# Kernel tuning notes

Measured on AMD Instinct MI355X. Metric: run time of the kernel, lower is better.

The kernel has to match this reference:

```python
import jax, jax.numpy as jnp
import numpy as np

V, E = 50000, 800000
NODE_IN, EDGE_IN, OUT, HEADS = 128, 16, 32, 4
NEG_SLOPE = 0.2  # DGL EdgeGATConv default negative_slope


def setup_inputs() -> dict:
    key = jax.random.key(0)
    ks = jax.random.split(key, 10)
    return {
        "node_feats": jax.random.normal(ks[0], (V, NODE_IN), jnp.float32),
        "edge_feats": jax.random.normal(ks[1], (E, EDGE_IN), jnp.float32),
        "src": jax.random.randint(ks[2], (E,), 0, V),
        "dst": jax.random.randint(ks[3], (E,), 0, V),
        "W_node": jax.random.normal(ks[4], (NODE_IN, HEADS * OUT), jnp.float32) * 0.05,
        "W_edge": jax.random.normal(ks[5], (EDGE_IN, HEADS * OUT), jnp.float32) * 0.05,
        "attn_l": jax.random.normal(ks[6], (HEADS, OUT), jnp.float32) * 0.05,
        "attn_r": jax.random.normal(ks[7], (HEADS, OUT), jnp.float32) * 0.05,
        "attn_e": jax.random.normal(ks[8], (HEADS, OUT), jnp.float32) * 0.05,
        "res_W": jax.random.normal(ks[9], (NODE_IN, HEADS * OUT), jnp.float32) * 0.05,
        "bias": jnp.zeros((HEADS * OUT,), jnp.float32),
    }


def _leaky_relu(x, slope):
    return jnp.where(x >= 0, x, slope * x)


def reference(node_feats, edge_feats, src, dst, W_node, W_edge, attn_l, attn_r, attn_e, res_W, bias):
    V = node_feats.shape[0]
    H, F = attn_l.shape
    # linear projections
    ft = (node_feats @ W_node).reshape(V, H, F)    # [V,H,F]
    fe = (edge_feats @ W_edge).reshape(-1, H, F)   # [E,H,F]
    # per-head attention logits
    el = jnp.einsum('vhf,hf->vh', ft, attn_l)      # [V,H]
    er = jnp.einsum('vhf,hf->vh', ft, attn_r)      # [V,H]
    ee = jnp.einsum('ehf,hf->eh', fe, attn_e)      # [E,H]
    e = _leaky_relu(el[src] + er[dst] + ee, NEG_SLOPE)  # [E,H]
    # edge softmax over incoming edges of each destination node (stable)
    emax = jax.ops.segment_max(e, dst, num_segments=V)  # [V,H]
    ex = jnp.exp(e - emax[dst])
    esum = jax.ops.segment_sum(ex, dst, num_segments=V)  # [V,H]
    a = ex / esum[dst]                                   # [E,H]
    # weighted message passing: u_mul_e(ft, a) then sum to dst
    msg = ft[src] * a[:, :, None]                        # [E,H,F]
    rst = jax.ops.segment_sum(msg, dst, num_segments=V)  # [V,H,F]
    # residual connection + bias (EdgeGATConv residual=True, bias=True)
    rst = rst + (node_feats @ res_W).reshape(V, H, F)
    rst = rst + bias.reshape(1, H, F)
    # agg_mode='flatten': concat heads
    return rst.reshape(V, H * F)
```

## Files before the change

kernel.cpp:

```cpp
#include <hip/hip_runtime.h>
#include <hip/hip_fp16.h>
#include <cstdint>

#define V_N 50000
#define E_N 800000
#define NODE_IN 128
#define EDGE_IN 16
#define HF 128
#define NEG_SLOPE 0.2f
#define NB_SCAN 196

#define OFF_FT    0
#define OFF_EL    3200000
#define OFF_ER    3400000
#define OFF_DEG   3600000
#define OFF_ROW   3650000
#define OFF_BSUM  3700004
#define OFF_RANK  3700260
#define OFF_REC   4500260
#define OFF_WATT  7700260
#define OFF_BFRAG 7700324

typedef short bf16x8 __attribute__((ext_vector_type(8)));
typedef float f32x4 __attribute__((ext_vector_type(4)));

__device__ __forceinline__ unsigned short f2bf(float f) {
    unsigned u = __float_as_uint(f);
    u += 0x7fffu + ((u >> 16) & 1u);
    return (unsigned short)(u >> 16);
}
__device__ __forceinline__ unsigned pk2(float lo, float hi) {
    return (unsigned)f2bf(lo) | ((unsigned)f2bf(hi) << 16);
}
__device__ __forceinline__ float bflo(unsigned w) { return __uint_as_float(w << 16); }
__device__ __forceinline__ float bfhi(unsigned w) { return __uint_as_float(w & 0xffff0000u); }

typedef __fp16 fp16x2 __attribute__((ext_vector_type(2)));
__device__ __forceinline__ unsigned pkh2(float a, float b) {
    fp16x2 h = __builtin_amdgcn_cvt_pkrtz(a, b);
    return __builtin_bit_cast(unsigned, h);
}
__device__ __forceinline__ __half2 u2h(unsigned u) {
    return __builtin_bit_cast(__half2, u);
}
__device__ __forceinline__ unsigned h2u(__half2 h) {
    return __builtin_bit_cast(unsigned, h);
}

__global__ void k_prep(const float* __restrict__ We,
                       const float* __restrict__ attn_e,
                       const float* __restrict__ Wn,
                       const float* __restrict__ Wr,
                       float* __restrict__ watt,
                       unsigned* __restrict__ bfrag,
                       int* __restrict__ deg) {
    int g = blockIdx.x * 256 + threadIdx.x;
    for (int i = g; i < V_N; i += 16384) deg[i] = 0;
    if (blockIdx.x == 0 && threadIdx.x < 64) {
        int k = threadIdx.x >> 2, h = threadIdx.x & 3;
        float s = 0.f;
        #pragma unroll
        for (int f = 0; f < 32; f++)
            s += We[k * HF + h * 32 + f] * attn_e[h * 32 + f];
        watt[k * 4 + h] = s;
    }
    if (g < 16384) {
        int c    = g >> 8;
        int lane = (g >> 2) & 63;
        int jp   = g & 3;
        int nt = c >> 2, ks = c & 3;
        int col = nt * 16 + (lane & 15);
        int k   = ks * 32 + (lane >> 4) * 8 + jp * 2;
        const float* W = (col < 128) ? Wn : Wr;
        int cc = col & 127;
        float x0 = W[(size_t)k * 128 + cc];
        float x1 = W[(size_t)(k + 1) * 128 + cc];
        bfrag[g] = pk2(x0, x1);
    }
}

__global__ __launch_bounds__(256) void k_node(
    const float* __restrict__ nf, const unsigned* __restrict__ bfragw,
    const float* __restrict__ attn_l, const float* __restrict__ attn_r,
    const float* __restrict__ bias,
    unsigned short* __restrict__ ftw, float* __restrict__ el,
    float* __restrict__ er, float* __restrict__ out)
{
    __shared__ __align__(16) float sSf[32 * 140];
    unsigned short* sA = (unsigned short*)sSf;

    const int t = threadIdx.x;
    const int lane = t & 63;
    const int w = t >> 6;
    const int nb = blockIdx.x * 32;
    const int n15 = lane & 15;
    const int q = lane >> 4;
    const unsigned short* bfrag = (const unsigned short*)bfragw;

    #pragma unroll
    for (int i = 0; i < 4; i++) {
        int f = t + i * 256;
        int node = f >> 5;
        int kc = (f & 31) * 4;
        float4 v = {0.f, 0.f, 0.f, 0.f};
        if (nb + node < V_N)
            v = *(const float4*)(nf + (size_t)(nb + node) * NODE_IN + kc);
        uint2 u2 = make_uint2(pk2(v.x, v.y), pk2(v.z, v.w));
        *(uint2*)&sA[node * 136 + kc] = u2;
    }
    __syncthreads();

    f32x4 acc[2][4];
    #pragma unroll
    for (int m = 0; m < 2; m++)
        #pragma unroll
        for (int tt = 0; tt < 4; tt++) acc[m][tt] = (f32x4){0.f, 0.f, 0.f, 0.f};

    #pragma unroll
    for (int ks = 0; ks < 4; ks++) {
        bf16x8 a0 = *(const bf16x8*)&sA[n15 * 136 + ks * 32 + q * 8];
        bf16x8 a1 = *(const bf16x8*)&sA[(16 + n15) * 136 + ks * 32 + q * 8];
        #pragma unroll
        for (int tt = 0; tt < 4; tt++) {
            int nt = w * 4 + tt;
            bf16x8 b = *(const bf16x8*)(bfrag + ((size_t)(nt * 4 + ks) * 64 + lane) * 8);
            acc[0][tt] = __builtin_amdgcn_mfma_f32_16x16x32_bf16(a0, b, acc[0][tt], 0, 0, 0);
            acc[1][tt] = __builtin_amdgcn_mfma_f32_16x16x32_bf16(a1, b, acc[1][tt], 0, 0, 0);
        }
    }

    if (w < 2) {
        #pragma unroll
        for (int hh = 0; hh < 2; hh++) {
            int head = w * 2 + hh;
            float al0 = attn_l[head * 32 + n15];
            float al1 = attn_l[head * 32 + 16 + n15];
            float ar0 = attn_r[head * 32 + n15];
            float ar1 = attn_r[head * 32 + 16 + n15];
            #pragma unroll
            for (int m = 0; m < 2; m++) {
                #pragma unroll
                for (int r = 0; r < 4; r++) {
                    float fa = acc[m][hh * 2][r], fb = acc[m][hh * 2 + 1][r];
                    float elp = fa * al0 + fb * al1;
                    float erp = fa * ar0 + fb * ar1;
                    elp += __shfl_xor(elp, 1); erp += __shfl_xor(erp, 1);
                    elp += __shfl_xor(elp, 2); erp += __shfl_xor(erp, 2);
                    elp += __shfl_xor(elp, 4); erp += __shfl_xor(erp, 4);
                    elp += __shfl_xor(elp, 8); erp += __shfl_xor(erp, 8);
                    int node = nb + m * 16 + q * 4 + r;
                    if (n15 == 0 && node < V_N) {
                        el[node * 4 + head] = elp;
                        er[node * 4 + head] = erp;
                    }
                }
            }
        }
        #pragma unroll
        for (int m = 0; m < 2; m++)
            #pragma unroll
            for (int r = 0; r < 4; r++) {
                int node = nb + m * 16 + q * 4 + r;
                if (node < V_N) {
                    uint2 u;
                    u.x = pkh2(acc[m][0][r], acc[m][1][r]);
                    u.y = pkh2(acc[m][2][r], acc[m][3][r]);
                    *(uint2*)(ftw + (size_t)node * 128 + w * 64 + n15 * 4) = u;
                }
            }
    }
    __syncthreads();

    if (w >= 2) {
        #pragma unroll
        for (int m = 0; m < 2; m++)
            #pragma unroll
            for (int tt = 0; tt < 4; tt++)
                #pragma unroll
                for (int r = 0; r < 4; r++)
                    sSf[(m * 16 + q * 4 + r) * 140 + (w - 2) * 64 + tt * 16 + n15] =
                        acc[m][tt][r];
    }
    __syncthreads();
    #pragma unroll
    for (int i = 0; i < 4; i++) {
        int u = t + i * 256;
        int node = u >> 5, c4 = (u & 31) * 4;
        if (nb + node < V_N) {
            float4 v = *(float4*)&sSf[node * 140 + c4];
            float4 b4 = *(const float4*)(bias + c4);
            v.x += b4.x; v.y += b4.y; v.z += b4.z; v.w += b4.w;
            *(float4*)(out + (size_t)(nb + node) * HF + c4) = v;
        }
    }
}

__global__ void k_hist(const int* __restrict__ dst, int* __restrict__ deg,
                       int* __restrict__ rank) {
    int e = blockIdx.x * 256 + threadIdx.x;
    if (e < E_N) rank[e] = atomicAdd(&deg[dst[e]], 1);
}

__global__ __launch_bounds__(256) void k_scan1(const int* __restrict__ deg,
                                               int* __restrict__ rowp,
                                               int* __restrict__ bsum) {
    __shared__ int sh[256];
    int t = threadIdx.x, b = blockIdx.x;
    int i = b * 256 + t;
    int v = (i < V_N) ? deg[i] : 0;
    sh[t] = v;
    __syncthreads();
    #pragma unroll
    for (int off = 1; off < 256; off <<= 1) {
        int u = (t >= off) ? sh[t - off] : 0;
        __syncthreads();
        sh[t] += u;
        __syncthreads();
    }
    if (i < V_N) rowp[i] = sh[t] - v;
    if (t == 255) bsum[b] = sh[255];
}

__global__ __launch_bounds__(256) void k_scan23(int* __restrict__ rowp,
                                                const int* __restrict__ bsum) {
    __shared__ int sh[256];
    int t = threadIdx.x, b = blockIdx.x;
    int v = (t < NB_SCAN) ? bsum[t] : 0;
    sh[t] = v;
    __syncthreads();
    #pragma unroll
    for (int off = 1; off < 256; off <<= 1) {
        int u = (t >= off) ? sh[t - off] : 0;
        __syncthreads();
        sh[t] += u;
        __syncthreads();
    }
    int boff = (b == 0) ? 0 : sh[b - 1];
    int i = b * 256 + t;
    if (i < V_N) rowp[i] += boff;
    if (i == 0) rowp[V_N] = E_N;
}

__global__ __launch_bounds__(256) void k_escatter(
    const float* __restrict__ ef, const int* __restrict__ src,
    const int* __restrict__ dst, const int* __restrict__ rank,
    const int* __restrict__ rowp, const float* __restrict__ watt,
    uint4* __restrict__ rec)
{
    __shared__ float sw[64];
    if (threadIdx.x < 64) sw[threadIdx.x] = watt[threadIdx.x];
    __syncthreads();
    int e = blockIdx.x * 256 + threadIdx.x;
    if (e >= E_N) return;

    float eev[4] = {0.f, 0.f, 0.f, 0.f};
    #pragma unroll
    for (int kq = 0; kq < 4; kq++) {
        float4 v = *(const float4*)(ef + (size_t)e * EDGE_IN + kq * 4);
        float vv[4] = {v.x, v.y, v.z, v.w};
        #pragma unroll
        for (int j = 0; j < 4; j++) {
            int k = kq * 4 + j;
            #pragma unroll
            for (int h = 0; h < 4; h++) eev[h] += vv[j] * sw[k * 4 + h];
        }
    }
    int d = dst[e];
    int p = rowp[d] + rank[e];
    uint4 r;
    r.x = (unsigned)src[e];
    r.y = pk2(eev[0], eev[1]);
    r.z = pk2(eev[2], eev[3]);
    r.w = 0;
    rec[p] = r;
}

__global__ __launch_bounds__(256) void k_gather(
    const int* __restrict__ row, const uint4* __restrict__ rec,
    const float* __restrict__ el, const float* __restrict__ er,
    const unsigned short* __restrict__ ftw, float* __restrict__ out)
{
    __shared__ unsigned aw[4][64][4];
    const int lane = threadIdx.x & 63;
    const int wid  = threadIdx.x >> 6;
    const int d = blockIdx.x * 4 + wid;
    if (d >= V_N) return;
    const int n0 = row[d];
    const int deg = row[d + 1] - n0;
    if (deg == 0) return;

    float4 er4 = *(const float4*)(er + (size_t)d * 4);

    int   si0 = 0;
    float4 ex0 = {0.f, 0.f, 0.f, 0.f};
    float4 s4  = {0.f, 0.f, 0.f, 0.f};
    for (int i = lane; i < deg; i += 64) {
        uint4 r = rec[n0 + i];
        float4 el4 = *(const float4*)(el + (size_t)r.x * 4);
        float x0 = el4.x + er4.x + bflo(r.y);
        float x1 = el4.y + er4.y + bfhi(r.y);
        float x2 = el4.z + er4.z + bflo(r.z);
        float x3 = el4.w + er4.w + bfhi(r.z);
        x0 = x0 >= 0.f ? x0 : NEG_SLOPE * x0;
        x1 = x1 >= 0.f ? x1 : NEG_SLOPE * x1;
        x2 = x2 >= 0.f ? x2 : NEG_SLOPE * x2;
        x3 = x3 >= 0.f ? x3 : NEG_SLOPE * x3;
        float4 ex = {__expf(x0), __expf(x1), __expf(x2), __expf(x3)};
        if (i == lane) { si0 = (int)r.x; ex0 = ex; }
        s4.x += ex.x; s4.y += ex.y; s4.z += ex.z; s4.w += ex.w;
    }
    #pragma unroll
    for (int off = 1; off < 64; off <<= 1) {
        s4.x += __shfl_xor(s4.x, off);
        s4.y += __shfl_xor(s4.y, off);
        s4.z += __shfl_xor(s4.z, off);
        s4.w += __shfl_xor(s4.w, off);
    }
    float4 rs4 = {1.f / s4.x, 1.f / s4.y, 1.f / s4.z, 1.f / s4.w};

    const int qw = lane >> 4, li = lane & 15;
    const int wsel = li >> 3;
    __half2 hacc0 = u2h(0u), hacc1 = u2h(0u), hacc2 = u2h(0u), hacc3 = u2h(0u);

    for (int i0 = 0; i0 < deg; i0 += 64) {
        int chunk = min(64, deg - i0);
        int si = 0;
        float4 a4 = {0.f, 0.f, 0.f, 0.f};
        if (lane < chunk) {
            if (i0 == 0) {
                si = si0;
                a4.x = ex0.x * rs4.x; a4.y = ex0.y * rs4.y;
                a4.z = ex0.z * rs4.z; a4.w = ex0.w * rs4.w;
            } else {
                uint4 r = rec[n0 + i0 + lane];
                si = (int)r.x;
                float4 el4 = *(const float4*)(el + (size_t)r.x * 4);
                float x0 = el4.x + er4.x + bflo(r.y);
                float x1 = el4.y + er4.y + bfhi(r.y);
                float x2 = el4.z + er4.z + bflo(r.z);
                float x3 = el4.w + er4.w + bfhi(r.z);
                x0 = x0 >= 0.f ? x0 : NEG_SLOPE * x0;
                x1 = x1 >= 0.f ? x1 : NEG_SLOPE * x1;
                x2 = x2 >= 0.f ? x2 : NEG_SLOPE * x2;
                x3 = x3 >= 0.f ? x3 : NEG_SLOPE * x3;
                a4.x = __expf(x0) * rs4.x; a4.y = __expf(x1) * rs4.y;
                a4.z = __expf(x2) * rs4.z; a4.w = __expf(x3) * rs4.w;
            }
        }
        uint4 ap;
        ap.x = pkh2(a4.x, a4.x); ap.y = pkh2(a4.y, a4.y);
        ap.z = pkh2(a4.z, a4.z); ap.w = pkh2(a4.w, a4.w);
        *(uint4*)&aw[wid][lane][0] = ap;
        asm volatile("s_waitcnt lgkmcnt(0)" ::: "memory");

        int iters = (chunk + 3) & ~3;
        for (int j = 0; j < iters; j += 4) {
            int jq = j + qw;
            int sidx = __shfl(si, jq);
            uint2 au = *(const uint2*)&aw[wid][jq][wsel * 2];
            uint4 wv = *(const uint4*)(ftw + (size_t)sidx * 128 + li * 8);
            hacc0 = __hfma2(u2h(wv.x), u2h(au.x), hacc0);
            hacc1 = __hfma2(u2h(wv.y), u2h(au.y), hacc1);
            hacc2 = __hfma2(u2h(wv.z), u2h(au.x), hacc2);
            hacc3 = __hfma2(u2h(wv.w), u2h(au.y), hacc3);
        }
    }
    hacc0 = __hadd2(hacc0, u2h(__shfl_xor(h2u(hacc0), 16)));
    hacc1 = __hadd2(hacc1, u2h(__shfl_xor(h2u(hacc1), 16)));
    hacc2 = __hadd2(hacc2, u2h(__shfl_xor(h2u(hacc2), 16)));
    hacc3 = __hadd2(hacc3, u2h(__shfl_xor(h2u(hacc3), 16)));
    hacc0 = __hadd2(hacc0, u2h(__shfl_xor(h2u(hacc0), 32)));
    hacc1 = __hadd2(hacc1, u2h(__shfl_xor(h2u(hacc1), 32)));
    hacc2 = __hadd2(hacc2, u2h(__shfl_xor(h2u(hacc2), 32)));
    hacc3 = __hadd2(hacc3, u2h(__shfl_xor(h2u(hacc3), 32)));
    if (qw == 0) {
        float* op = out + (size_t)d * HF + wsel * 64 + (li & 7) * 2;
        float2 r;
        r = *(float2*)(op +  0); r.x += __low2float(hacc0);  r.y += __low2float(hacc2);  *(float2*)(op +  0) = r;
        r = *(float2*)(op + 16); r.x += __high2float(hacc0); r.y += __high2float(hacc2); *(float2*)(op + 16) = r;
        r = *(float2*)(op + 32); r.x += __low2float(hacc1);  r.y += __low2float(hacc3);  *(float2*)(op + 32) = r;
        r = *(float2*)(op + 48); r.x += __high2float(hacc1); r.y += __high2float(hacc3); *(float2*)(op + 48) = r;
    }
}

extern "C" void kernel_launch(void* const* d_in, const int* in_sizes, int n_in,
                              void* d_out, int out_size, void* d_ws, size_t ws_size,
                              hipStream_t stream) {
    const float* nf     = (const float*)d_in[0];
    const float* ef     = (const float*)d_in[1];
    const int*   src    = (const int*)d_in[2];
    const int*   dst    = (const int*)d_in[3];
    const float* Wn     = (const float*)d_in[4];
    const float* We     = (const float*)d_in[5];
    const float* attn_l = (const float*)d_in[6];
    const float* attn_r = (const float*)d_in[7];
    const float* attn_e = (const float*)d_in[8];
    const float* Wr     = (const float*)d_in[9];
    const float* bias   = (const float*)d_in[10];
    float* out = (float*)d_out;

    unsigned* wsw  = (unsigned*)d_ws;
    unsigned short* ftw = (unsigned short*)(wsw + OFF_FT);
    float* el      = (float*)(wsw + OFF_EL);
    float* er      = (float*)(wsw + OFF_ER);
    int* deg       = (int*)(wsw + OFF_DEG);
    int* rowp      = (int*)(wsw + OFF_ROW);
    int* bsum      = (int*)(wsw + OFF_BSUM);
    int* rank      = (int*)(wsw + OFF_RANK);
    uint4* rec     = (uint4*)(wsw + OFF_REC);
    float* watt    = (float*)(wsw + OFF_WATT);
    unsigned* bfrag = wsw + OFF_BFRAG;

    k_prep<<<64, 256, 0, stream>>>(We, attn_e, Wn, Wr, watt, bfrag, deg);
    k_hist<<<(E_N + 255) / 256, 256, 0, stream>>>(dst, deg, rank);
    k_scan1<<<NB_SCAN, 256, 0, stream>>>(deg, rowp, bsum);
    k_scan23<<<NB_SCAN, 256, 0, stream>>>(rowp, bsum);
    k_escatter<<<(E_N + 255) / 256, 256, 0, stream>>>(ef, src, dst, rank,
                                                      rowp, watt, rec);
    k_node<<<(V_N + 31) / 32, 256, 0, stream>>>(nf, bfrag, attn_l, attn_r,
                                                bias, ftw, el, er, out);
    k_gather<<<(V_N + 3) / 4, 256, 0, stream>>>(rowp, rec, el, er, ftw, out);
}
```

Before: 248.9 us.

## Precompute exp attention logits in edge scatter and dual-accumulate gather loop

Moves the leaky-relu and exp of the attention logits from the gather kernel into the edge scatter kernel, which now runs after the node kernel so el/er are available. Each edge record stores bf16 exp values, so the gather no longer makes random el loads or recomputes exp in both passes. The gather inner loop is also unrolled to two independent half2 accumulator sets to expose more memory-level parallelism. The softmax is now computed without max subtraction directly in bf16-packed exp values, which relies on logits staying small (the original also lacked max subtraction), and the scatter kernel now does random el/er loads instead.

```diff
diff --git a/kernel.cpp b/kernel.cpp
--- a/kernel.cpp
+++ b/kernel.cpp
@@ -245,6 +245,7 @@
     const float* __restrict__ ef, const int* __restrict__ src,
     const int* __restrict__ dst, const int* __restrict__ rank,
     const int* __restrict__ rowp, const float* __restrict__ watt,
+    const float* __restrict__ el, const float* __restrict__ er,
     uint4* __restrict__ rec)
 {
     __shared__ float sw[64];
@@ -265,19 +266,28 @@
             for (int h = 0; h < 4; h++) eev[h] += vv[j] * sw[k * 4 + h];
         }
     }
-    int d = dst[e];
+    int s = src[e], d = dst[e];
+    float4 el4 = *(const float4*)(el + (size_t)s * 4);
+    float4 er4 = *(const float4*)(er + (size_t)d * 4);
+    float x0 = el4.x + er4.x + eev[0];
+    float x1 = el4.y + er4.y + eev[1];
+    float x2 = el4.z + er4.z + eev[2];
+    float x3 = el4.w + er4.w + eev[3];
+    x0 = x0 >= 0.f ? x0 : NEG_SLOPE * x0;
+    x1 = x1 >= 0.f ? x1 : NEG_SLOPE * x1;
+    x2 = x2 >= 0.f ? x2 : NEG_SLOPE * x2;
+    x3 = x3 >= 0.f ? x3 : NEG_SLOPE * x3;
     int p = rowp[d] + rank[e];
     uint4 r;
-    r.x = (unsigned)src[e];
-    r.y = pk2(eev[0], eev[1]);
-    r.z = pk2(eev[2], eev[3]);
+    r.x = (unsigned)s;
+    r.y = pk2(__expf(x0), __expf(x1));
+    r.z = pk2(__expf(x2), __expf(x3));
     r.w = 0;
     rec[p] = r;
 }
 
 __global__ __launch_bounds__(256) void k_gather(
     const int* __restrict__ row, const uint4* __restrict__ rec,
-    const float* __restrict__ el, const float* __restrict__ er,
     const unsigned short* __restrict__ ftw, float* __restrict__ out)
 {
     __shared__ unsigned aw[4][64][4];
@@ -289,23 +299,12 @@
     const int deg = row[d + 1] - n0;
     if (deg == 0) return;
 
-    float4 er4 = *(const float4*)(er + (size_t)d * 4);
-
     int   si0 = 0;
     float4 ex0 = {0.f, 0.f, 0.f, 0.f};
     float4 s4  = {0.f, 0.f, 0.f, 0.f};
     for (int i = lane; i < deg; i += 64) {
         uint4 r = rec[n0 + i];
-        float4 el4 = *(const float4*)(el + (size_t)r.x * 4);
-        float x0 = el4.x + er4.x + bflo(r.y);
-        float x1 = el4.y + er4.y + bfhi(r.y);
-        float x2 = el4.z + er4.z + bflo(r.z);
-        float x3 = el4.w + er4.w + bfhi(r.z);
-        x0 = x0 >= 0.f ? x0 : NEG_SLOPE * x0;
-        x1 = x1 >= 0.f ? x1 : NEG_SLOPE * x1;
-        x2 = x2 >= 0.f ? x2 : NEG_SLOPE * x2;
-        x3 = x3 >= 0.f ? x3 : NEG_SLOPE * x3;
-        float4 ex = {__expf(x0), __expf(x1), __expf(x2), __expf(x3)};
+        float4 ex = {bflo(r.y), bfhi(r.y), bflo(r.z), bfhi(r.z)};
         if (i == lane) { si0 = (int)r.x; ex0 = ex; }
         s4.x += ex.x; s4.y += ex.y; s4.z += ex.z; s4.w += ex.w;
     }
@@ -320,7 +319,8 @@
 
     const int qw = lane >> 4, li = lane & 15;
     const int wsel = li >> 3;
-    __half2 hacc0 = u2h(0u), hacc1 = u2h(0u), hacc2 = u2h(0u), hacc3 = u2h(0u);
+    __half2 ha0 = u2h(0u), ha1 = u2h(0u), ha2 = u2h(0u), ha3 = u2h(0u);
+    __half2 hb0 = u2h(0u), hb1 = u2h(0u), hb2 = u2h(0u), hb3 = u2h(0u);
 
     for (int i0 = 0; i0 < deg; i0 += 64) {
         int chunk = min(64, deg - i0);
@@ -334,17 +334,8 @@
             } else {
                 uint4 r = rec[n0 + i0 + lane];
                 si = (int)r.x;
-                float4 el4 = *(const float4*)(el + (size_t)r.x * 4);
-                float x0 = el4.x + er4.x + bflo(r.y);
-                float x1 = el4.y + er4.y + bfhi(r.y);
-                float x2 = el4.z + er4.z + bflo(r.z);
-                float x3 = el4.w + er4.w + bfhi(r.z);
-                x0 = x0 >= 0.f ? x0 : NEG_SLOPE * x0;
-                x1 = x1 >= 0.f ? x1 : NEG_SLOPE * x1;
-                x2 = x2 >= 0.f ? x2 : NEG_SLOPE * x2;
-                x3 = x3 >= 0.f ? x3 : NEG_SLOPE * x3;
-                a4.x = __expf(x0) * rs4.x; a4.y = __expf(x1) * rs4.y;
-                a4.z = __expf(x2) * rs4.z; a4.w = __expf(x3) * rs4.w;
+                a4.x = bflo(r.y) * rs4.x; a4.y = bfhi(r.y) * rs4.y;
+                a4.z = bflo(r.z) * rs4.z; a4.w = bfhi(r.z) * rs4.w;
             }
         }
         uint4 ap;
@@ -353,33 +344,42 @@
         *(uint4*)&aw[wid][lane][0] = ap;
         asm volatile("s_waitcnt lgkmcnt(0)" ::: "memory");
 
-        int iters = (chunk + 3) & ~3;
-        for (int j = 0; j < iters; j += 4) {
-            int jq = j + qw;
-            int sidx = __shfl(si, jq);
-            uint2 au = *(const uint2*)&aw[wid][jq][wsel * 2];
-            uint4 wv = *(const uint4*)(ftw + (size_t)sidx * 128 + li * 8);
-            hacc0 = __hfma2(u2h(wv.x), u2h(au.x), hacc0);
-            hacc1 = __hfma2(u2h(wv.y), u2h(au.y), hacc1);
-            hacc2 = __hfma2(u2h(wv.z), u2h(au.x), hacc2);
-            hacc3 = __hfma2(u2h(wv.w), u2h(au.y), hacc3);
-        }
-    }
-    hacc0 = __hadd2(hacc0, u2h(__shfl_xor(h2u(hacc0), 16)));
-    hacc1 = __hadd2(hacc1, u2h(__shfl_xor(h2u(hacc1), 16)));
-    hacc2 = __hadd2(hacc2, u2h(__shfl_xor(h2u(hacc2), 16)));
-    hacc3 = __hadd2(hacc3, u2h(__shfl_xor(h2u(hacc3), 16)));
-    hacc0 = __hadd2(hacc0, u2h(__shfl_xor(h2u(hacc0), 32)));
-    hacc1 = __hadd2(hacc1, u2h(__shfl_xor(h2u(hacc1), 32)));
-    hacc2 = __hadd2(hacc2, u2h(__shfl_xor(h2u(hacc2), 32)));
-    hacc3 = __hadd2(hacc3, u2h(__shfl_xor(h2u(hacc3), 32)));
+        int iters = (chunk + 7) & ~7;
+        for (int j = 0; j < iters; j += 8) {
+            int jq0 = j + qw, jq1 = j + qw + 4;
+            int sidx0 = __shfl(si, jq0);
+            int sidx1 = __shfl(si, jq1);
+            uint2 au0 = *(const uint2*)&aw[wid][jq0][wsel * 2];
+            uint2 au1 = *(const uint2*)&aw[wid][jq1][wsel * 2];
+            uint4 wv0 = *(const uint4*)(ftw + (size_t)sidx0 * 128 + li * 8);
+            uint4 wv1 = *(const uint4*)(ftw + (size_t)sidx1 * 128 + li * 8);
+            ha0 = __hfma2(u2h(wv0.x), u2h(au0.x), ha0);
+            ha1 = __hfma2(u2h(wv0.y), u2h(au0.y), ha1);
+            ha2 = __hfma2(u2h(wv0.z), u2h(au0.x), ha2);
+            ha3 = __hfma2(u2h(wv0.w), u2h(au0.y), ha3);
+            hb0 = __hfma2(u2h(wv1.x), u2h(au1.x), hb0);
+            hb1 = __hfma2(u2h(wv1.y), u2h(au1.y), hb1);
+            hb2 = __hfma2(u2h(wv1.z), u2h(au1.x), hb2);
+            hb3 = __hfma2(u2h(wv1.w), u2h(au1.y), hb3);
+        }
+    }
+    ha0 = __hadd2(ha0, hb0); ha1 = __hadd2(ha1, hb1);
+    ha2 = __hadd2(ha2, hb2); ha3 = __hadd2(ha3, hb3);
+    ha0 = __hadd2(ha0, u2h(__shfl_xor(h2u(ha0), 16)));
+    ha1 = __hadd2(ha1, u2h(__shfl_xor(h2u(ha1), 16)));
+    ha2 = __hadd2(ha2, u2h(__shfl_xor(h2u(ha2), 16)));
+    ha3 = __hadd2(ha3, u2h(__shfl_xor(h2u(ha3), 16)));
+    ha0 = __hadd2(ha0, u2h(__shfl_xor(h2u(ha0), 32)));
+    ha1 = __hadd2(ha1, u2h(__shfl_xor(h2u(ha1), 32)));
+    ha2 = __hadd2(ha2, u2h(__shfl_xor(h2u(ha2), 32)));
+    ha3 = __hadd2(ha3, u2h(__shfl_xor(h2u(ha3), 32)));
     if (qw == 0) {
         float* op = out + (size_t)d * HF + wsel * 64 + (li & 7) * 2;
         float2 r;
-        r = *(float2*)(op +  0); r.x += __low2float(hacc0);  r.y += __low2float(hacc2);  *(float2*)(op +  0) = r;
-        r = *(float2*)(op + 16); r.x += __high2float(hacc0); r.y += __high2float(hacc2); *(float2*)(op + 16) = r;
-        r = *(float2*)(op + 32); r.x += __low2float(hacc1);  r.y += __low2float(hacc3);  *(float2*)(op + 32) = r;
-        r = *(float2*)(op + 48); r.x += __high2float(hacc1); r.y += __high2float(hacc3); *(float2*)(op + 48) = r;
+        r = *(float2*)(op +  0); r.x += __low2float(ha0);  r.y += __low2float(ha2);  *(float2*)(op +  0) = r;
+        r = *(float2*)(op + 16); r.x += __high2float(ha0); r.y += __high2float(ha2); *(float2*)(op + 16) = r;
+        r = *(float2*)(op + 32); r.x += __low2float(ha1);  r.y += __low2float(ha3);  *(float2*)(op + 32) = r;
+        r = *(float2*)(op + 48); r.x += __high2float(ha1); r.y += __high2float(ha3); *(float2*)(op + 48) = r;
     }
 }
 
@@ -415,9 +415,9 @@
     k_hist<<<(E_N + 255) / 256, 256, 0, stream>>>(dst, deg, rank);
     k_scan1<<<NB_SCAN, 256, 0, stream>>>(deg, rowp, bsum);
     k_scan23<<<NB_SCAN, 256, 0, stream>>>(rowp, bsum);
-    k_escatter<<<(E_N + 255) / 256, 256, 0, stream>>>(ef, src, dst, rank,
-                                                      rowp, watt, rec);
     k_node<<<(V_N + 31) / 32, 256, 0, stream>>>(nf, bfrag, attn_l, attn_r,
                                                 bias, ftw, el, er, out);
-    k_gather<<<(V_N + 3) / 4, 256, 0, stream>>>(rowp, rec, el, er, ftw, out);
-}
+    k_escatter<<<(E_N + 255) / 256, 256, 0, stream>>>(ef, src, dst, rank,
+                                                      rowp, watt, el, er, rec);
+    k_gather<<<(V_N + 3) / 4, 256, 0, stream>>>(rowp, rec, ftw, out);
+}
```

Measured after the change: 252.4 us. About the same (+1.4%).
